# Performance work log

Hardware: AMD Instinct MI355X
Metric: run time of the kernel (lower is better)

## Reference

```python
import math
import jax, jax.numpy as jnp
import numpy as np

DIM = 256
HEADS = 8
WS = (8, 8)   # window_size
SS = (4, 4)   # shift_size


def _rel_tables():
    """Static SwinV2 continuous relative-position coordinate table and index."""
    wh, ww = WS
    ch = np.arange(-(wh - 1), wh, dtype=np.float32)
    cw = np.arange(-(ww - 1), ww, dtype=np.float32)
    table = np.stack(np.meshgrid(ch, cw, indexing='ij'), axis=-1)  # (2wh-1, 2ww-1, 2)
    table[..., 0] /= (wh - 1)
    table[..., 1] /= (ww - 1)
    table *= 8.0
    table = np.sign(table) * np.log2(np.abs(table) + 1.0) / 3.0
    coords = np.stack(np.meshgrid(np.arange(wh), np.arange(ww), indexing='ij'))
    cf = coords.reshape(2, -1)                      # (2, N)
    rel = (cf[:, :, None] - cf[:, None, :]).transpose(1, 2, 0)  # (N, N, 2)
    rel[..., 0] += wh - 1
    rel[..., 1] += ww - 1
    rel[..., 0] *= 2 * ww - 1
    idx = rel.sum(-1).reshape(-1)                   # (N*N,)
    return jnp.asarray(table, jnp.float32), jnp.asarray(idx, jnp.int32)


def _attn_mask(pad_H, pad_W, sh, sw):
    """Static shifted-window attention mask, shape (num_windows, N, N)."""
    wh, ww = WS
    m = np.zeros((pad_H, pad_W), np.float32)
    cnt = 0
    for hs in ((0, -wh), (-wh, -sh), (-sh, None)):
        for ws_ in ((0, -ww), (-ww, -sw), (-sw, None)):
            m[hs[0]:hs[1], ws_[0]:ws_[1]] = cnt
            cnt += 1
    m = m.reshape(pad_H // wh, wh, pad_W // ww, ww).transpose(0, 2, 1, 3)
    m = m.reshape(-1, wh * ww)                      # (nW, N)
    diff = m[:, None, :] - m[:, :, None]            # (nW, N, N)
    return jnp.asarray(np.where(diff != 0, -100.0, 0.0).astype(np.float32))


def setup_inputs() -> dict:
    key = jax.random.key(0)
    ks = jax.random.split(key, 12)
    C, Hh = DIM, HEADS
    s = 0.02
    inp = {
        'x': jax.random.normal(ks[0], (16, 64, 64, C), jnp.float32),
        'Wq': jax.random.normal(ks[1], (C, C), jnp.float32) * s,
        'bq': jnp.zeros((C,), jnp.float32),
        'Wk': jax.random.normal(ks[2], (C, C), jnp.float32) * s,
        'bk': jnp.zeros((C,), jnp.float32),
        'Wv': jax.random.normal(ks[3], (C, C), jnp.float32) * s,
        'bv': jnp.zeros((C,), jnp.float32),
        'Wo': jax.random.normal(ks[4], (C, C), jnp.float32) * s,
        'bo': jnp.zeros((C,), jnp.float32),
        'logit_scale': jnp.full((Hh, 1, 1), math.log(10.0), jnp.float32),
        'cpb_w1': jax.random.normal(ks[5], (2, 512), jnp.float32) * s,
        'cpb_b1': jnp.zeros((512,), jnp.float32),
        'cpb_w2': jax.random.normal(ks[6], (512, Hh), jnp.float32) * s,
    }
    return inp


def reference(x, Wq, bq, Wk, bk, Wv, bv, Wo, bo, logit_scale, cpb_w1, cpb_b1, cpb_w2):
    B, H, W, C = x.shape
    wh, ww = WS
    hd = C // HEADS
    pad_b = (wh - H % wh) % wh
    pad_r = (ww - W % ww) % ww
    x = jnp.pad(x, ((0, 0), (0, pad_b), (0, pad_r), (0, 0)))
    pH, pW = H + pad_b, W + pad_r
    sh = 0 if wh >= pH else SS[0]
    sw = 0 if ww >= pW else SS[1]

    xs = jnp.roll(x, (-sh, -sw), axis=(1, 2))
    nW = (pH // wh) * (pW // ww)
    N = wh * ww
    # window partition -> (B*nW, N, C)
    xw = xs.reshape(B, pH // wh, wh, pW // ww, ww, C).transpose(0, 1, 3, 2, 4, 5)
    xw = xw.reshape(B * nW, N, C)

    def heads(t):
        return t.reshape(B * nW, N, HEADS, hd).transpose(0, 2, 1, 3)  # (BnW, H, N, hd)

    q = heads(xw @ Wq + bq)
    k = heads(xw @ Wk + bk)
    v = heads(xw @ Wv + bv)

    # cosine attention (F.normalize, eps=1e-12)
    qn = q / jnp.maximum(jnp.linalg.norm(q, axis=-1, keepdims=True), 1e-12)
    kn = k / jnp.maximum(jnp.linalg.norm(k, axis=-1, keepdims=True), 1e-12)
    attn = jnp.einsum('bhnd,bhmd->bhnm', qn, kn)

    scale = jnp.exp(jnp.minimum(logit_scale, math.log(100.0)))  # (HEADS,1,1)
    attn = attn * scale[None]

    table, idx = _rel_tables()
    bias = jax.nn.relu(table @ cpb_w1 + cpb_b1) @ cpb_w2        # (2wh-1, 2ww-1, HEADS)
    bias = bias.reshape(-1, HEADS)[idx].reshape(N, N, HEADS).transpose(2, 0, 1)
    attn = attn + (16.0 * jax.nn.sigmoid(bias))[None]

    if sh + sw > 0:
        mask = _attn_mask(pH, pW, sh, sw)                        # (nW, N, N)
        attn = attn.reshape(B, nW, HEADS, N, N) + mask[None, :, None]
        attn = attn.reshape(B * nW, HEADS, N, N)

    attn = jax.nn.softmax(attn, axis=-1)
    out = jnp.einsum('bhnm,bhmd->bhnd', attn, v)
    out = out.transpose(0, 2, 1, 3).reshape(B * nW, N, C)
    out = out @ Wo + bo

    out = out.reshape(B, pH // wh, pW // ww, wh, ww, C).transpose(0, 1, 3, 2, 4, 5)
    out = out.reshape(B, pH, pW, C)
    if sh + sw > 0:
        out = jnp.roll(out, (sh, sw), axis=(1, 2))
    return out[:, :H, :W, :]
```

## Files before the change

### kernel.cpp

```cpp
#include <hip/hip_runtime.h>
#include <hip/hip_bf16.h>

typedef float floatx4 __attribute__((ext_vector_type(4)));
typedef short shortx8 __attribute__((ext_vector_type(8)));
typedef short shortx4 __attribute__((ext_vector_type(4)));

#define CFENCE() asm volatile("" ::: "memory")

__device__ __forceinline__ float bf2f(short s) {
    union { unsigned u; float f; } cv;
    cv.u = ((unsigned)(unsigned short)s) << 16;
    return cv.f;
}
__device__ __forceinline__ short f2bf(float f) {
    union { float f; unsigned u; } cv; cv.f = f;
    unsigned r = (cv.u + 0x7fffu + ((cv.u >> 16) & 1u)) >> 16;
    return (short)r;
}

__global__ __launch_bounds__(256) void wtrans(const float* __restrict__ Wq,
                                              const float* __restrict__ Wk,
                                              const float* __restrict__ Wv,
                                              const float* __restrict__ Wo,
                                              short* __restrict__ wqkv_f,
                                              short* __restrict__ wo_f) {
    int gtid = blockIdx.x * 256 + threadIdx.x;
    int f = gtid >> 6, lane = gtid & 63;
    int quad = lane >> 4, l15 = lane & 15;
    if (f < 384) {
        int n16 = f >> 3, kt = f & 7;
        int n = n16 * 16 + l15, z = n >> 8, ncol = n & 255;
        const float* src = (z == 0) ? Wq : (z == 1) ? Wk : Wv;
        shortx8 s;
#pragma unroll
        for (int j = 0; j < 8; ++j)
            s[j] = f2bf(src[(size_t)(kt * 32 + quad * 8 + j) * 256 + ncol]);
        *(shortx8*)(wqkv_f + (size_t)f * 512 + lane * 8) = s;
    } else {
        int f2 = f - 384;
        int n16 = f2 >> 3, kt = f2 & 7;
        int n = n16 * 16 + l15;
        shortx8 s;
#pragma unroll
        for (int j = 0; j < 8; ++j)
            s[j] = f2bf(Wo[(size_t)(kt * 32 + quad * 8 + j) * 256 + n]);
        *(shortx8*)(wo_f + (size_t)f2 * 512 + lane * 8) = s;
    }
}

__device__ __forceinline__ float sgnlog(float x) {
    return copysignf(__log2f(fabsf(x) + 1.f) / 3.f, x);
}
__global__ __launch_bounds__(256) void bias_mlp(const float* __restrict__ ls,
                                                const float* __restrict__ w1,
                                                const float* __restrict__ b1,
                                                const float* __restrict__ w2,
                                                float* __restrict__ b225g,
                                                float* __restrict__ scaleOut) {
    int e = blockIdx.x;
    int tid = threadIdx.x, lane = tid & 63, wid = tid >> 6;
    if (e == 0 && tid < 8) scaleOut[tid] = expf(fminf(ls[tid], 4.6051701859880914f));
    int dh = e / 15 - 7, dw = e % 15 - 7;
    float t0 = sgnlog(8.f * (float)dh / 7.f);
    float t1 = sgnlog(8.f * (float)dw / 7.f);
    float acc[8];
#pragma unroll
    for (int j = 0; j < 8; ++j) acc[j] = 0.f;
#pragma unroll
    for (int s = 0; s < 2; ++s) {
        int hsm = tid + s * 256;
        float hid = fmaxf(0.f, t0 * w1[hsm] + t1 * w1[512 + hsm] + b1[hsm]);
#pragma unroll
        for (int j = 0; j < 8; ++j) acc[j] += hid * w2[hsm * 8 + j];
    }
#pragma unroll
    for (int off = 1; off < 64; off <<= 1)
#pragma unroll
        for (int j = 0; j < 8; ++j) acc[j] += __shfl_xor(acc[j], off, 64);
    __shared__ float red[4][8];
    if (lane == 0)
#pragma unroll
        for (int j = 0; j < 8; ++j) red[wid][j] = acc[j];
    __syncthreads();
    if (tid < 8)
        b225g[e * 8 + tid] = red[0][tid] + red[1][tid] + red[2][tid] + red[3][tid];
}

__global__ __launch_bounds__(256) void bias_expand(const float* __restrict__ b225g,
                                                   float* __restrict__ bias_t) {
    int f = blockIdx.x * 256 + threadIdx.x;
    int h = f >> 12, ij = f & 4095, i = ij >> 6, j = ij & 63;
    int dh = (i >> 3) - (j >> 3), dw = (i & 7) - (j & 7);
    int e = (dh + 7) * 15 + (dw + 7);
    float v = b225g[e * 8 + h];
    bias_t[(h << 12) + j * 64 + i] = 16.f / (1.f + expf(-v));
}

__device__ __forceinline__ int row2pix(int row) {
    int w = row >> 6, t = row & 63;
    int b = w >> 6, wi = (w >> 3) & 7, wj = w & 7;
    int hh = (wi * 8 + (t >> 3) + 4) & 63;
    int ww = (wj * 8 + (t & 7) + 4) & 63;
    return (b * 64 + hh) * 64 + ww;
}

__device__ __forceinline__ int regid(int t, int wi, int wj) {
    int a = (wi < 7) ? 0 : (((t >> 3) < 4) ? 1 : 2);
    int b = (wj < 7) ? 0 : (((t & 7) < 4) ? 1 : 2);
    return a * 3 + b;
}

__global__ __launch_bounds__(256) void xtrans(const float* __restrict__ x,
                                              short* __restrict__ xbf) {
    int win = blockIdx.x;
    int tid = threadIdx.x;
    int r = tid >> 2, q = tid & 3;
    const float* src = x + (size_t)row2pix(win * 64 + r) * 256 + q * 64;
    size_t fb = (size_t)(win * 4 + (r >> 4)) * 8;
    int l15r = r & 15;
#pragma unroll
    for (int kt2 = 0; kt2 < 2; ++kt2) {
        int kt = q * 2 + kt2;
        short* dst = xbf + (fb + kt) * 512 + l15r * 8;
#pragma unroll
        for (int quad = 0; quad < 4; ++quad) {
            float4 u0 = *(const float4*)(src + kt2 * 32 + quad * 8);
            float4 u1 = *(const float4*)(src + kt2 * 32 + quad * 8 + 4);
            shortx8 t;
            t[0] = f2bf(u0.x); t[1] = f2bf(u0.y); t[2] = f2bf(u0.z); t[3] = f2bf(u0.w);
            t[4] = f2bf(u1.x); t[5] = f2bf(u1.y); t[6] = f2bf(u1.z); t[7] = f2bf(u1.w);
            *(shortx8*)(dst + quad * 128) = t;
        }
    }
}

__global__ __launch_bounds__(256, 2) void swin_fused(const short* __restrict__ xbf,
                                                     const short* __restrict__ wf,
                                                     const short* __restrict__ wof,
                                                     const float* __restrict__ bq,
                                                     const float* __restrict__ bk_,
                                                     const float* __restrict__ bv,
                                                     const float* __restrict__ bo,
                                                     const float* __restrict__ bias_t,
                                                     const float* __restrict__ scale,
                                                     float* __restrict__ out) {
    __shared__ __align__(16) short lds[26112];
    int tid = threadIdx.x, lane = tid & 63, wid = tid >> 6;
    int quad = lane >> 4, l15 = lane & 15;
    int win = blockIdx.x;
    int wi = (win >> 3) & 7, wj = win & 7;
    bool need_mask = (wi == 7) || (wj == 7);

    short* qn = &lds[wid * 6528];
    short* kn = qn + 2176;
    short* vt = qn + 4352;
    short* P  = qn;

    const short* xfb = xbf + (size_t)(win * 4) * 8 * 512 + lane * 8;

    shortx4 Obf[2][4][2];

#pragma unroll
    for (int p = 0; p < 2; ++p) {
        int h = wid * 2 + p;
        float sc = scale[h];
        floatx4 aq[2][4], ak[2][4];
#pragma unroll
        for (int i = 0; i < 2; ++i)
#pragma unroll
            for (int mt = 0; mt < 4; ++mt) {
                aq[i][mt] = (floatx4){0.f, 0.f, 0.f, 0.f};
                ak[i][mt] = (floatx4){0.f, 0.f, 0.f, 0.f};
            }
#pragma unroll
        for (int kt = 0; kt < 8; ++kt) {
            shortx8 af[4];
#pragma unroll
            for (int mt = 0; mt < 4; ++mt)
                af[mt] = *(const shortx8*)(xfb + (size_t)(mt * 8 + kt) * 512);
            shortx8 wqf[2], wkf[2];
#pragma unroll
            for (int i = 0; i < 2; ++i) {
                int n16 = 2 * h + i;
                wqf[i] = *(const shortx8*)(wf + (size_t)((n16)*8 + kt) * 512 + lane * 8);
                wkf[i] = *(const shortx8*)(wf + (size_t)((16 + n16) * 8 + kt) * 512 + lane * 8);
            }
#pragma unroll
            for (int i = 0; i < 2; ++i)
#pragma unroll
                for (int mt = 0; mt < 4; ++mt) {
                    aq[i][mt] = __builtin_amdgcn_mfma_f32_16x16x32_bf16(wqf[i], af[mt], aq[i][mt], 0, 0, 0);
                    ak[i][mt] = __builtin_amdgcn_mfma_f32_16x16x32_bf16(wkf[i], af[mt], ak[i][mt], 0, 0, 0);
                }
        }
        float qs[4], ks[4];
#pragma unroll
        for (int mt = 0; mt < 4; ++mt) { qs[mt] = 0.f; ks[mt] = 0.f; }
#pragma unroll
        for (int i = 0; i < 2; ++i) {
            float bqv[4], bkv[4];
#pragma unroll
            for (int r = 0; r < 4; ++r) {
                int d = i * 16 + quad * 4 + r;
                bqv[r] = bq[h * 32 + d];
                bkv[r] = bk_[h * 32 + d];
            }
#pragma unroll
            for (int mt = 0; mt < 4; ++mt)
#pragma unroll
                for (int r = 0; r < 4; ++r) {
                    float qv = aq[i][mt][r] + bqv[r]; aq[i][mt][r] = qv; qs[mt] += qv * qv;
                    float kv = ak[i][mt][r] + bkv[r]; ak[i][mt][r] = kv; ks[mt] += kv * kv;
                }
        }
#pragma unroll
        for (int mt = 0; mt < 4; ++mt) {
            qs[mt] += __shfl_xor(qs[mt], 16, 64); qs[mt] += __shfl_xor(qs[mt], 32, 64);
            ks[mt] += __shfl_xor(ks[mt], 16, 64); ks[mt] += __shfl_xor(ks[mt], 32, 64);
        }
        CFENCE();
#pragma unroll
        for (int mt = 0; mt < 4; ++mt) {
            float qr = sc / fmaxf(sqrtf(qs[mt]), 1e-12f);
            float kr = 1.f / fmaxf(sqrtf(ks[mt]), 1e-12f);
            int tok = mt * 16 + l15;
#pragma unroll
            for (int i = 0; i < 2; ++i) {
                shortx4 oq, ok;
#pragma unroll
                for (int r = 0; r < 4; ++r) {
                    oq[r] = f2bf(aq[i][mt][r] * qr);
                    ok[r] = f2bf(ak[i][mt][r] * kr);
                }
                *(shortx4*)&qn[tok * 34 + i * 16 + quad * 4] = oq;
                *(shortx4*)&kn[tok * 34 + i * 16 + quad * 4] = ok;
            }
        }
        CFENCE();
        floatx4 av[2][4];
#pragma unroll
        for (int i = 0; i < 2; ++i)
#pragma unroll
            for (int mt = 0; mt < 4; ++mt) av[i][mt] = (floatx4){0.f, 0.f, 0.f, 0.f};
#pragma unroll
        for (int kt = 0; kt < 8; ++kt) {
            shortx8 af[4];
#pragma unroll
            for (int mt = 0; mt < 4; ++mt)
                af[mt] = *(const shortx8*)(xfb + (size_t)(mt * 8 + kt) * 512);
            shortx8 wvf[2];
#pragma unroll
            for (int i = 0; i < 2; ++i) {
                int n16 = 2 * h + i;
                wvf[i] = *(const shortx8*)(wf + (size_t)((32 + n16) * 8 + kt) * 512 + lane * 8);
            }
#pragma unroll
            for (int i = 0; i < 2; ++i)
#pragma unroll
                for (int mt = 0; mt < 4; ++mt)
                    av[i][mt] = __builtin_amdgcn_mfma_f32_16x16x32_bf16(wvf[i], af[mt], av[i][mt], 0, 0, 0);
        }
#pragma unroll
        for (int i = 0; i < 2; ++i) {
            float bvv[4];
#pragma unroll
            for (int r = 0; r < 4; ++r) bvv[r] = bv[h * 32 + i * 16 + quad * 4 + r];
#pragma unroll
            for (int mt = 0; mt < 4; ++mt) {
                int tok = mt * 16 + l15;
#pragma unroll
                for (int r = 0; r < 4; ++r)
                    vt[(i * 16 + quad * 4 + r) * 68 + tok] = f2bf(av[i][mt][r] + bvv[r]);
            }
        }
        CFENCE();
        shortx8 aqf[4], bkf[4];
#pragma unroll
        for (int mt = 0; mt < 4; ++mt)
            aqf[mt] = *(const shortx8*)&qn[(mt * 16 + l15) * 34 + quad * 8];
#pragma unroll
        for (int nt = 0; nt < 4; ++nt)
            bkf[nt] = *(const shortx8*)&kn[(nt * 16 + l15) * 34 + quad * 8];
        floatx4 S[4][4];
#pragma unroll
        for (int mt = 0; mt < 4; ++mt)
#pragma unroll
            for (int nt = 0; nt < 4; ++nt) {
                floatx4 z = {0.f, 0.f, 0.f, 0.f};
                S[mt][nt] = __builtin_amdgcn_mfma_f32_16x16x32_bf16(aqf[mt], bkf[nt], z, 0, 0, 0);
            }
        const float* bh = bias_t + (h << 12);
        float bound = sc + 16.5f;
        int jid[4];
        if (need_mask) {
#pragma unroll
            for (int nt = 0; nt < 4; ++nt) jid[nt] = regid(nt * 16 + l15, wi, wj);
        }
        float rs[4][4];
#pragma unroll
        for (int mt = 0; mt < 4; ++mt) {
            float4 b4[4];
#pragma unroll
            for (int nt = 0; nt < 4; ++nt)
                b4[nt] = *(const float4*)&bh[(nt * 16 + l15) * 64 + mt * 16 + quad * 4];
#pragma unroll
            for (int reg = 0; reg < 4; ++reg) {
                int i = mt * 16 + quad * 4 + reg;
                int iid = need_mask ? regid(i, wi, wj) : 0;
                float rowsum = 0.f;
#pragma unroll
                for (int nt = 0; nt < 4; ++nt) {
                    float bb = (reg == 0) ? b4[nt].x : (reg == 1) ? b4[nt].y
                             : (reg == 2) ? b4[nt].z : b4[nt].w;
                    float v = S[mt][nt][reg] + bb;
                    if (need_mask && iid != jid[nt]) v -= 100.f;
                    float pe = __expf(v - bound);
                    S[mt][nt][reg] = pe;
                    rowsum += pe;
                }
                rowsum += __shfl_xor(rowsum, 1, 64);
                rowsum += __shfl_xor(rowsum, 2, 64);
                rowsum += __shfl_xor(rowsum, 4, 64);
                rowsum += __shfl_xor(rowsum, 8, 64);
                rs[mt][reg] = 1.f / rowsum;
            }
        }
        CFENCE();
#pragma unroll
        for (int mt = 0; mt < 4; ++mt)
#pragma unroll
            for (int nt = 0; nt < 4; ++nt)
#pragma unroll
                for (int reg = 0; reg < 4; ++reg)
                    P[(mt * 16 + quad * 4 + reg) * 68 + nt * 16 + l15] = f2bf(S[mt][nt][reg]);
        CFENCE();
        floatx4 O[4][2];
#pragma unroll
        for (int mt = 0; mt < 4; ++mt)
#pragma unroll
            for (int nt = 0; nt < 2; ++nt) O[mt][nt] = (floatx4){0.f, 0.f, 0.f, 0.f};
#pragma unroll
        for (int ks2 = 0; ks2 < 2; ++ks2) {
            shortx8 pa[4], vb[2];
#pragma unroll
            for (int mt = 0; mt < 4; ++mt)
                pa[mt] = *(const shortx8*)&P[(mt * 16 + l15) * 68 + ks2 * 32 + quad * 8];
#pragma unroll
            for (int nt = 0; nt < 2; ++nt)
                vb[nt] = *(const shortx8*)&vt[(nt * 16 + l15) * 68 + ks2 * 32 + quad * 8];
#pragma unroll
            for (int mt = 0; mt < 4; ++mt)
#pragma unroll
                for (int nt = 0; nt < 2; ++nt)
                    O[mt][nt] = __builtin_amdgcn_mfma_f32_16x16x32_bf16(pa[mt], vb[nt], O[mt][nt], 0, 0, 0);
        }
#pragma unroll
        for (int mt = 0; mt < 4; ++mt)
#pragma unroll
            for (int nt = 0; nt < 2; ++nt) {
                shortx4 s;
#pragma unroll
                for (int reg = 0; reg < 4; ++reg)
                    s[reg] = f2bf(O[mt][nt][reg] * rs[mt][reg]);
                Obf[p][mt][nt] = s;
            }
        CFENCE();
    }

    __syncthreads();
    short* Ao = lds;
#pragma unroll
    for (int p = 0; p < 2; ++p) {
        int h = wid * 2 + p;
#pragma unroll
        for (int mt = 0; mt < 4; ++mt)
#pragma unroll
            for (int nt = 0; nt < 2; ++nt)
#pragma unroll
                for (int reg = 0; reg < 4; ++reg)
                    Ao[(mt * 16 + quad * 4 + reg) * 264 + h * 32 + nt * 16 + l15] =
                        Obf[p][mt][nt][reg];
    }
    __syncthreads();

    int pix[4];
#pragma unroll
    for (int mt = 0; mt < 4; ++mt) pix[mt] = row2pix(win * 64 + mt * 16 + l15);

    floatx4 acc2[4][4];
#pragma unroll
    for (int nt = 0; nt < 4; ++nt)
#pragma unroll
        for (int mt = 0; mt < 4; ++mt) acc2[nt][mt] = (floatx4){0.f, 0.f, 0.f, 0.f};
#pragma unroll
    for (int kt = 0; kt < 8; ++kt) {
        shortx8 bw[4], af2[4];
#pragma unroll
        for (int nt = 0; nt < 4; ++nt)
            bw[nt] = *(const shortx8*)(wof + (size_t)((wid * 4 + nt) * 8 + kt) * 512 + lane * 8);
#pragma unroll
        for (int mt = 0; mt < 4; ++mt)
            af2[mt] = *(const shortx8*)&Ao[(mt * 16 + l15) * 264 + kt * 32 + quad * 8];
#pragma unroll
        for (int nt = 0; nt < 4; ++nt)
#pragma unroll
            for (int mt = 0; mt < 4; ++mt)
                acc2[nt][mt] = __builtin_amdgcn_mfma_f32_16x16x32_bf16(bw[nt], af2[mt], acc2[nt][mt], 0, 0, 0);
    }
#pragma unroll
    for (int nt = 0; nt < 4; ++nt) {
        int nb = wid * 64 + nt * 16 + quad * 4;
        float bs[4];
#pragma unroll
        for (int reg = 0; reg < 4; ++reg) bs[reg] = bo[nb + reg];
#pragma unroll
        for (int mt = 0; mt < 4; ++mt) {
            float4 o;
            o.x = acc2[nt][mt][0] + bs[0];
            o.y = acc2[nt][mt][1] + bs[1];
            o.z = acc2[nt][mt][2] + bs[2];
            o.w = acc2[nt][mt][3] + bs[3];
            *(float4*)(out + (size_t)pix[mt] * 256 + nb) = o;
        }
    }
}

extern "C" void kernel_launch(void* const* d_in, const int* in_sizes, int n_in,
                              void* d_out, int out_size, void* d_ws, size_t ws_size,
                              hipStream_t stream) {
    const float* x  = (const float*)d_in[0];
    const float* Wq = (const float*)d_in[1];
    const float* bq = (const float*)d_in[2];
    const float* Wk = (const float*)d_in[3];
    const float* bk = (const float*)d_in[4];
    const float* Wv = (const float*)d_in[5];
    const float* bv = (const float*)d_in[6];
    const float* Wo = (const float*)d_in[7];
    const float* bo = (const float*)d_in[8];
    const float* ls = (const float*)d_in[9];
    const float* w1 = (const float*)d_in[10];
    const float* b1 = (const float*)d_in[11];
    const float* w2 = (const float*)d_in[12];

    char* ws = (char*)d_ws;
    short* wqkv_f = (short*)(ws + 0);
    short* wo_f   = (short*)(ws + 393216);
    float* bias_t = (float*)(ws + 524288);
    float* scale  = (float*)(ws + 655360);
    float* b225g  = (float*)(ws + 786432);
    short* xbf    = (short*)(ws + 1048576);
    float* out    = (float*)d_out;

    hipLaunchKernelGGL(wtrans, dim3(128), dim3(256), 0, stream, Wq, Wk, Wv, Wo, wqkv_f, wo_f);
    hipLaunchKernelGGL(bias_mlp, dim3(225), dim3(256), 0, stream, ls, w1, b1, w2, b225g, scale);
    hipLaunchKernelGGL(bias_expand, dim3(128), dim3(256), 0, stream, b225g, bias_t);
    hipLaunchKernelGGL(xtrans, dim3(1024), dim3(256), 0, stream, x, xbf);
    hipLaunchKernelGGL(swin_fused, dim3(1024), dim3(256), 0, stream,
                       xbf, wqkv_f, wo_f, bq, bk, bv, bo, bias_t, scale, out);
}
```

Measured before the change: 241.0 us.

## Fuse x bf16 conversion into attention kernel and use one wave per head

```diff
diff --git a/kernel.cpp b/kernel.cpp
--- a/kernel.cpp
+++ b/kernel.cpp
@@ -110,31 +110,7 @@
     return a * 3 + b;
 }
 
-__global__ __launch_bounds__(256) void xtrans(const float* __restrict__ x,
-                                              short* __restrict__ xbf) {
-    int win = blockIdx.x;
-    int tid = threadIdx.x;
-    int r = tid >> 2, q = tid & 3;
-    const float* src = x + (size_t)row2pix(win * 64 + r) * 256 + q * 64;
-    size_t fb = (size_t)(win * 4 + (r >> 4)) * 8;
-    int l15r = r & 15;
-#pragma unroll
-    for (int kt2 = 0; kt2 < 2; ++kt2) {
-        int kt = q * 2 + kt2;
-        short* dst = xbf + (fb + kt) * 512 + l15r * 8;
-#pragma unroll
-        for (int quad = 0; quad < 4; ++quad) {
-            float4 u0 = *(const float4*)(src + kt2 * 32 + quad * 8);
-            float4 u1 = *(const float4*)(src + kt2 * 32 + quad * 8 + 4);
-            shortx8 t;
-            t[0] = f2bf(u0.x); t[1] = f2bf(u0.y); t[2] = f2bf(u0.z); t[3] = f2bf(u0.w);
-            t[4] = f2bf(u1.x); t[5] = f2bf(u1.y); t[6] = f2bf(u1.z); t[7] = f2bf(u1.w);
-            *(shortx8*)(dst + quad * 128) = t;
-        }
-    }
-}
-
-__global__ __launch_bounds__(256, 2) void swin_fused(const short* __restrict__ xbf,
+__global__ __launch_bounds__(512, 2) void swin_fused(const float* __restrict__ x,
                                                      const short* __restrict__ wf,
                                                      const short* __restrict__ wof,
                                                      const float* __restrict__ bq,
@@ -144,272 +120,279 @@
                                                      const float* __restrict__ bias_t,
                                                      const float* __restrict__ scale,
                                                      float* __restrict__ out) {
-    __shared__ __align__(16) short lds[26112];
+    __shared__ __align__(16) short lds[68608];
     int tid = threadIdx.x, lane = tid & 63, wid = tid >> 6;
     int quad = lane >> 4, l15 = lane & 15;
     int win = blockIdx.x;
     int wi = (win >> 3) & 7, wj = win & 7;
     bool need_mask = (wi == 7) || (wj == 7);
 
-    short* qn = &lds[wid * 6528];
+    short* xtile = lds;
+    short* qn = &lds[16384 + wid * 6528];
     short* kn = qn + 2176;
     short* vt = qn + 4352;
     short* P  = qn;
 
-    const short* xfb = xbf + (size_t)(win * 4) * 8 * 512 + lane * 8;
-
-    shortx4 Obf[2][4][2];
-
-#pragma unroll
-    for (int p = 0; p < 2; ++p) {
-        int h = wid * 2 + p;
-        float sc = scale[h];
-        floatx4 aq[2][4], ak[2][4];
+    {
+        int r = tid >> 3, seg = tid & 7;
+        const float* src = x + (size_t)row2pix(win * 64 + r) * 256 + seg * 32;
+        short* dst = &xtile[((r >> 4) * 8 + seg) * 512 + (r & 15) * 8];
+#pragma unroll
+        for (int c4 = 0; c4 < 4; ++c4) {
+            float4 u0 = *(const float4*)(src + c4 * 8);
+            float4 u1 = *(const float4*)(src + c4 * 8 + 4);
+            shortx8 t;
+            t[0] = f2bf(u0.x); t[1] = f2bf(u0.y); t[2] = f2bf(u0.z); t[3] = f2bf(u0.w);
+            t[4] = f2bf(u1.x); t[5] = f2bf(u1.y); t[6] = f2bf(u1.z); t[7] = f2bf(u1.w);
+            *(shortx8*)(dst + c4 * 128) = t;
+        }
+    }
+    __syncthreads();
+
+    int h = wid;
+    float sc = scale[h];
+
+    floatx4 aq[2][4], ak[2][4];
+#pragma unroll
+    for (int i = 0; i < 2; ++i)
+#pragma unroll
+        for (int mt = 0; mt < 4; ++mt) {
+            aq[i][mt] = (floatx4){0.f, 0.f, 0.f, 0.f};
+            ak[i][mt] = (floatx4){0.f, 0.f, 0.f, 0.f};
+        }
+#pragma unroll
+    for (int kt = 0; kt < 8; ++kt) {
+        shortx8 af[4];
+#pragma unroll
+        for (int mt = 0; mt < 4; ++mt)
+            af[mt] = *(const shortx8*)&xtile[(mt * 8 + kt) * 512 + lane * 8];
+        shortx8 wqf[2], wkf[2];
+#pragma unroll
+        for (int i = 0; i < 2; ++i) {
+            int n16 = 2 * h + i;
+            wqf[i] = *(const shortx8*)(wf + (size_t)((n16)*8 + kt) * 512 + lane * 8);
+            wkf[i] = *(const shortx8*)(wf + (size_t)((16 + n16) * 8 + kt) * 512 + lane * 8);
+        }
 #pragma unroll
         for (int i = 0; i < 2; ++i)
 #pragma unroll
             for (int mt = 0; mt < 4; ++mt) {
-                aq[i][mt] = (floatx4){0.f, 0.f, 0.f, 0.f};
-                ak[i][mt] = (floatx4){0.f, 0.f, 0.f, 0.f};
+                aq[i][mt] = __builtin_amdgcn_mfma_f32_16x16x32_bf16(wqf[i], af[mt], aq[i][mt], 0, 0, 0);
+                ak[i][mt] = __builtin_amdgcn_mfma_f32_16x16x32_bf16(wkf[i], af[mt], ak[i][mt], 0, 0, 0);
             }
-#pragma unroll
-        for (int kt = 0; kt < 8; ++kt) {
-            shortx8 af[4];
+    }
+    float qs[4], ks[4];
+#pragma unroll
+    for (int mt = 0; mt < 4; ++mt) { qs[mt] = 0.f; ks[mt] = 0.f; }
+#pragma unroll
+    for (int i = 0; i < 2; ++i) {
+        float bqv[4], bkv[4];
+#pragma unroll
+        for (int r = 0; r < 4; ++r) {
+            int d = i * 16 + quad * 4 + r;
+            bqv[r] = bq[h * 32 + d];
+            bkv[r] = bk_[h * 32 + d];
+        }
+#pragma unroll
+        for (int mt = 0; mt < 4; ++mt)
+#pragma unroll
+            for (int r = 0; r < 4; ++r) {
+                float qv = aq[i][mt][r] + bqv[r]; aq[i][mt][r] = qv; qs[mt] += qv * qv;
+                float kv = ak[i][mt][r] + bkv[r]; ak[i][mt][r] = kv; ks[mt] += kv * kv;
+            }
+    }
+#pragma unroll
+    for (int mt = 0; mt < 4; ++mt) {
+        qs[mt] += __shfl_xor(qs[mt], 16, 64); qs[mt] += __shfl_xor(qs[mt], 32, 64);
+        ks[mt] += __shfl_xor(ks[mt], 16, 64); ks[mt] += __shfl_xor(ks[mt], 32, 64);
+    }
+    CFENCE();
+#pragma unroll
+    for (int mt = 0; mt < 4; ++mt) {
+        float qr = sc / fmaxf(sqrtf(qs[mt]), 1e-12f);
+        float kr = 1.f / fmaxf(sqrtf(ks[mt]), 1e-12f);
+        int tok = mt * 16 + l15;
+#pragma unroll
+        for (int i = 0; i < 2; ++i) {
+            shortx4 oq, ok;
+#pragma unroll
+            for (int r = 0; r < 4; ++r) {
+                oq[r] = f2bf(aq[i][mt][r] * qr);
+                ok[r] = f2bf(ak[i][mt][r] * kr);
+            }
+            *(shortx4*)&qn[tok * 34 + i * 16 + quad * 4] = oq;
+            *(shortx4*)&kn[tok * 34 + i * 16 + quad * 4] = ok;
+        }
+    }
+    CFENCE();
+    floatx4 av[2][4];
+#pragma unroll
+    for (int i = 0; i < 2; ++i)
+#pragma unroll
+        for (int mt = 0; mt < 4; ++mt) av[i][mt] = (floatx4){0.f, 0.f, 0.f, 0.f};
+#pragma unroll
+    for (int kt = 0; kt < 8; ++kt) {
+        shortx8 af[4];
+#pragma unroll
+        for (int mt = 0; mt < 4; ++mt)
+            af[mt] = *(const shortx8*)&xtile[(mt * 8 + kt) * 512 + lane * 8];
+        shortx8 wvf[2];
+#pragma unroll
+        for (int i = 0; i < 2; ++i) {
+            int n16 = 2 * h + i;
+            wvf[i] = *(const shortx8*)(wf + (size_t)((32 + n16) * 8 + kt) * 512 + lane * 8);
+        }
+#pragma unroll
+        for (int i = 0; i < 2; ++i)
 #pragma unroll
             for (int mt = 0; mt < 4; ++mt)
-                af[mt] = *(const shortx8*)(xfb + (size_t)(mt * 8 + kt) * 512);
-            shortx8 wqf[2], wkf[2];
-#pragma unroll
-            for (int i = 0; i < 2; ++i) {
-                int n16 = 2 * h + i;
-                wqf[i] = *(const shortx8*)(wf + (size_t)((n16)*8 + kt) * 512 + lane * 8);
-                wkf[i] = *(const shortx8*)(wf + (size_t)((16 + n16) * 8 + kt) * 512 + lane * 8);
+                av[i][mt] = __builtin_amdgcn_mfma_f32_16x16x32_bf16(wvf[i], af[mt], av[i][mt], 0, 0, 0);
+    }
+#pragma unroll
+    for (int i = 0; i < 2; ++i) {
+        float bvv[4];
+#pragma unroll
+        for (int r = 0; r < 4; ++r) bvv[r] = bv[h * 32 + i * 16 + quad * 4 + r];
+#pragma unroll
+        for (int mt = 0; mt < 4; ++mt) {
+            int tok = mt * 16 + l15;
+#pragma unroll
+            for (int r = 0; r < 4; ++r)
+                vt[(i * 16 + quad * 4 + r) * 68 + tok] = f2bf(av[i][mt][r] + bvv[r]);
+        }
+    }
+    CFENCE();
+    shortx8 aqf[4], bkf[4];
+#pragma unroll
+    for (int mt = 0; mt < 4; ++mt)
+        aqf[mt] = *(const shortx8*)&qn[(mt * 16 + l15) * 34 + quad * 8];
+#pragma unroll
+    for (int nt = 0; nt < 4; ++nt)
+        bkf[nt] = *(const shortx8*)&kn[(nt * 16 + l15) * 34 + quad * 8];
+    floatx4 S[4][4];
+#pragma unroll
+    for (int mt = 0; mt < 4; ++mt)
+#pragma unroll
+        for (int nt = 0; nt < 4; ++nt) {
+            floatx4 z = {0.f, 0.f, 0.f, 0.f};
+            S[mt][nt] = __builtin_amdgcn_mfma_f32_16x16x32_bf16(aqf[mt], bkf[nt], z, 0, 0, 0);
+        }
+    const float* bh = bias_t + (h << 12);
+    float bound = sc + 16.5f;
+    int jid[4];
+    if (need_mask) {
+#pragma unroll
+        for (int nt = 0; nt < 4; ++nt) jid[nt] = regid(nt * 16 + l15, wi, wj);
+    }
+    float rs[4][4];
+#pragma unroll
+    for (int mt = 0; mt < 4; ++mt) {
+        float4 b4[4];
+#pragma unroll
+        for (int nt = 0; nt < 4; ++nt)
+            b4[nt] = *(const float4*)&bh[(nt * 16 + l15) * 64 + mt * 16 + quad * 4];
+#pragma unroll
+        for (int reg = 0; reg < 4; ++reg) {
+            int i = mt * 16 + quad * 4 + reg;
+            int iid = need_mask ? regid(i, wi, wj) : 0;
+            float rowsum = 0.f;
+#pragma unroll
+            for (int nt = 0; nt < 4; ++nt) {
+                float bb = (reg == 0) ? b4[nt].x : (reg == 1) ? b4[nt].y
+                         : (reg == 2) ? b4[nt].z : b4[nt].w;
+                float v = S[mt][nt][reg] + bb;
+                if (need_mask && iid != jid[nt]) v -= 100.f;
+                float pe = __expf(v - bound);
+                S[mt][nt][reg] = pe;
+                rowsum += pe;
             }
-#pragma unroll
-            for (int i = 0; i < 2; ++i)
-#pragma unroll
-                for (int mt = 0; mt < 4; ++mt) {
-                    aq[i][mt] = __builtin_amdgcn_mfma_f32_16x16x32_bf16(wqf[i], af[mt], aq[i][mt], 0, 0, 0);
-                    ak[i][mt] = __builtin_amdgcn_mfma_f32_16x16x32_bf16(wkf[i], af[mt], ak[i][mt], 0, 0, 0);
-                }
-        }
-        float qs[4], ks[4];
-#pragma unroll
-        for (int mt = 0; mt < 4; ++mt) { qs[mt] = 0.f; ks[mt] = 0.f; }
-#pragma unroll
-        for (int i = 0; i < 2; ++i) {
-            float bqv[4], bkv[4];
-#pragma unroll
-            for (int r = 0; r < 4; ++r) {
-                int d = i * 16 + quad * 4 + r;
-                bqv[r] = bq[h * 32 + d];
-                bkv[r] = bk_[h * 32 + d];
-            }
-#pragma unroll
-            for (int mt = 0; mt < 4; ++mt)
-#pragma unroll
-                for (int r = 0; r < 4; ++r) {
-                    float qv = aq[i][mt][r] + bqv[r]; aq[i][mt][r] = qv; qs[mt] += qv * qv;
-                    float kv = ak[i][mt][r] + bkv[r]; ak[i][mt][r] = kv; ks[mt] += kv * kv;
-                }
-        }
-#pragma unroll
-        for (int mt = 0; mt < 4; ++mt) {
-            qs[mt] += __shfl_xor(qs[mt], 16, 64); qs[mt] += __shfl_xor(qs[mt], 32, 64);
-            ks[mt] += __shfl_xor(ks[mt], 16, 64); ks[mt] += __shfl_xor(ks[mt], 32, 64);
-        }
-        CFENCE();
-#pragma unroll
-        for (int mt = 0; mt < 4; ++mt) {
-            float qr = sc / fmaxf(sqrtf(qs[mt]), 1e-12f);
-            float kr = 1.f / fmaxf(sqrtf(ks[mt]), 1e-12f);
-            int tok = mt * 16 + l15;
-#pragma unroll
-            for (int i = 0; i < 2; ++i) {
-                shortx4 oq, ok;
-#pragma unroll
-                for (int r = 0; r < 4; ++r) {
-                    oq[r] = f2bf(aq[i][mt][r] * qr);
-                    ok[r] = f2bf(ak[i][mt][r] * kr);
-                }
-                *(shortx4*)&qn[tok * 34 + i * 16 + quad * 4] = oq;
-                *(shortx4*)&kn[tok * 34 + i * 16 + quad * 4] = ok;
-            }
-        }
-        CFENCE();
-        floatx4 av[2][4];
-#pragma unroll
-        for (int i = 0; i < 2; ++i)
-#pragma unroll
-            for (int mt = 0; mt < 4; ++mt) av[i][mt] = (floatx4){0.f, 0.f, 0.f, 0.f};
-#pragma unroll
-        for (int kt = 0; kt < 8; ++kt) {
-            shortx8 af[4];
-#pragma unroll
-            for (int mt = 0; mt < 4; ++mt)
-                af[mt] = *(const shortx8*)(xfb + (size_t)(mt * 8 + kt) * 512);
-            shortx8 wvf[2];
-#pragma unroll
-            for (int i = 0; i < 2; ++i) {
-                int n16 = 2 * h + i;
-                wvf[i] = *(const shortx8*)(wf + (size_t)((32 + n16) * 8 + kt) * 512 + lane * 8);
-            }
-#pragma unroll
-            for (int i = 0; i < 2; ++i)
-#pragma unroll
-                for (int mt = 0; mt < 4; ++mt)
-                    av[i][mt] = __builtin_amdgcn_mfma_f32_16x16x32_bf16(wvf[i], af[mt], av[i][mt], 0, 0, 0);
-        }
-#pragma unroll
-        for (int i = 0; i < 2; ++i) {
-            float bvv[4];
-#pragma unroll
-            for (int r = 0; r < 4; ++r) bvv[r] = bv[h * 32 + i * 16 + quad * 4 + r];
-#pragma unroll
-            for (int mt = 0; mt < 4; ++mt) {
-                int tok = mt * 16 + l15;
-#pragma unroll
-                for (int r = 0; r < 4; ++r)
-                    vt[(i * 16 + quad * 4 + r) * 68 + tok] = f2bf(av[i][mt][r] + bvv[r]);
-            }
-        }
-        CFENCE();
-        shortx8 aqf[4], bkf[4];
-#pragma unroll
-        for (int mt = 0; mt < 4; ++mt)
-            aqf[mt] = *(const shortx8*)&qn[(mt * 16 + l15) * 34 + quad * 8];
+            rowsum += __shfl_xor(rowsum, 1, 64);
+            rowsum += __shfl_xor(rowsum, 2, 64);
+            rowsum += __shfl_xor(rowsum, 4, 64);
+            rowsum += __shfl_xor(rowsum, 8, 64);
+            rs[mt][reg] = 1.f / rowsum;
+        }
+    }
+    CFENCE();
+#pragma unroll
+    for (int mt = 0; mt < 4; ++mt)
 #pragma unroll
         for (int nt = 0; nt < 4; ++nt)
-            bkf[nt] = *(const shortx8*)&kn[(nt * 16 + l15) * 34 + quad * 8];
-        floatx4 S[4][4];
-#pragma unroll
-        for (int mt = 0; mt < 4; ++mt)
-#pragma unroll
-            for (int nt = 0; nt < 4; ++nt) {
-                floatx4 z = {0.f, 0.f, 0.f, 0.f};
-                S[mt][nt] = __builtin_amdgcn_mfma_f32_16x16x32_bf16(aqf[mt], bkf[nt], z, 0, 0, 0);
-            }
-        const float* bh = bias_t + (h << 12);
-        float bound = sc + 16.5f;
-        int jid[4];
-        if (need_mask) {
-#pragma unroll
-            for (int nt = 0; nt < 4; ++nt) jid[nt] = regid(nt * 16 + l15, wi, wj);
-        }
-        float rs[4][4];
-#pragma unroll
-        for (int mt = 0; mt < 4; ++mt) {
-            float4 b4[4];
-#pragma unroll
-            for (int nt = 0; nt < 4; ++nt)
-                b4[nt] = *(const float4*)&bh[(nt * 16 + l15) * 64 + mt * 16 + quad * 4];
-#pragma unroll
-            for (int reg = 0; reg < 4; ++reg) {
-                int i = mt * 16 + quad * 4 + reg;
-                int iid = need_mask ? regid(i, wi, wj) : 0;
-                float rowsum = 0.f;
-#pragma unroll
-                for (int nt = 0; nt < 4; ++nt) {
-                    float bb = (reg == 0) ? b4[nt].x : (reg == 1) ? b4[nt].y
-                             : (reg == 2) ? b4[nt].z : b4[nt].w;
-                    float v = S[mt][nt][reg] + bb;
-                    if (need_mask && iid != jid[nt]) v -= 100.f;
-                    float pe = __expf(v - bound);
-                    S[mt][nt][reg] = pe;
-                    rowsum += pe;
-                }
-                rowsum += __shfl_xor(rowsum, 1, 64);
-                rowsum += __shfl_xor(rowsum, 2, 64);
-                rowsum += __shfl_xor(rowsum, 4, 64);
-                rowsum += __shfl_xor(rowsum, 8, 64);
-                rs[mt][reg] = 1.f / rowsum;
-            }
-        }
-        CFENCE();
-#pragma unroll
-        for (int mt = 0; mt < 4; ++mt)
-#pragma unroll
-            for (int nt = 0; nt < 4; ++nt)
-#pragma unroll
-                for (int reg = 0; reg < 4; ++reg)
-                    P[(mt * 16 + quad * 4 + reg) * 68 + nt * 16 + l15] = f2bf(S[mt][nt][reg]);
-        CFENCE();
-        floatx4 O[4][2];
-#pragma unroll
-        for (int mt = 0; mt < 4; ++mt)
-#pragma unroll
-            for (int nt = 0; nt < 2; ++nt) O[mt][nt] = (floatx4){0.f, 0.f, 0.f, 0.f};
-#pragma unroll
-        for (int ks2 = 0; ks2 < 2; ++ks2) {
-            shortx8 pa[4], vb[2];
-#pragma unroll
-            for (int mt = 0; mt < 4; ++mt)
-                pa[mt] = *(const shortx8*)&P[(mt * 16 + l15) * 68 + ks2 * 32 + quad * 8];
+#pragma unroll
+            for (int reg = 0; reg < 4; ++reg)
+                P[(mt * 16 + quad * 4 + reg) * 68 + nt * 16 + l15] = f2bf(S[mt][nt][reg]);
+    CFENCE();
+    floatx4 O[4][2];
+#pragma unroll
+    for (int mt = 0; mt < 4; ++mt)
+#pragma unroll
+        for (int nt = 0; nt < 2; ++nt) O[mt][nt] = (floatx4){0.f, 0.f, 0.f, 0.f};
+#pragma unroll
+    for (int ks2 = 0; ks2 < 2; ++ks2) {
+        shortx8 pa[4], vb[2];
+#pragma unroll
+        for (int mt = 0; mt < 4; ++mt)
+            pa[mt] = *(const shortx8*)&P[(mt * 16 + l15) * 68 + ks2 * 32 + quad * 8];
+#pragma unroll
+        for (int nt = 0; nt < 2; ++nt)
+            vb[nt] = *(const shortx8*)&vt[(nt * 16 + l15) * 68 + ks2 * 32 + quad * 8];
+#pragma unroll
+        for (int mt = 0; mt < 4; ++mt)
 #pragma unroll
             for (int nt = 0; nt < 2; ++nt)
-                vb[nt] = *(const shortx8*)&vt[(nt * 16 + l15) * 68 + ks2 * 32 + quad * 8];
-#pragma unroll
-            for (int mt = 0; mt < 4; ++mt)
-#pragma unroll
-                for (int nt = 0; nt < 2; ++nt)
-                    O[mt][nt] = __builtin_amdgcn_mfma_f32_16x16x32_bf16(pa[mt], vb[nt], O[mt][nt], 0, 0, 0);
-        }
-#pragma unroll
-        for (int mt = 0; mt < 4; ++mt)
-#pragma unroll
-            for (int nt = 0; nt < 2; ++nt) {
-                shortx4 s;
-#pragma unroll
-                for (int reg = 0; reg < 4; ++reg)
-                    s[reg] = f2bf(O[mt][nt][reg] * rs[mt][reg]);
-                Obf[p][mt][nt] = s;
-            }
-        CFENCE();
-    }
+                O[mt][nt] = __builtin_amdgcn_mfma_f32_16x16x32_bf16(pa[mt], vb[nt], O[mt][nt], 0, 0, 0);
+    }
+    shortx4 Obf[4][2];
+#pragma unroll
+    for (int mt = 0; mt < 4; ++mt)
+#pragma unroll
+        for (int nt = 0; nt < 2; ++nt) {
+            shortx4 s;
+#pragma unroll
+            for (int reg = 0; reg < 4; ++reg)
+                s[reg] = f2bf(O[mt][nt][reg] * rs[mt][reg]);
+            Obf[mt][nt] = s;
+        }
 
     __syncthreads();
     short* Ao = lds;
 #pragma unroll
-    for (int p = 0; p < 2; ++p) {
-        int h = wid * 2 + p;
-#pragma unroll
-        for (int mt = 0; mt < 4; ++mt)
-#pragma unroll
-            for (int nt = 0; nt < 2; ++nt)
-#pragma unroll
-                for (int reg = 0; reg < 4; ++reg)
-                    Ao[(mt * 16 + quad * 4 + reg) * 264 + h * 32 + nt * 16 + l15] =
-                        Obf[p][mt][nt][reg];
-    }
+    for (int mt = 0; mt < 4; ++mt)
+#pragma unroll
+        for (int nt = 0; nt < 2; ++nt)
+#pragma unroll
+            for (int reg = 0; reg < 4; ++reg)
+                Ao[(mt * 16 + quad * 4 + reg) * 264 + h * 32 + nt * 16 + l15] =
+                    Obf[mt][nt][reg];
     __syncthreads();
 
     int pix[4];
 #pragma unroll
     for (int mt = 0; mt < 4; ++mt) pix[mt] = row2pix(win * 64 + mt * 16 + l15);
 
-    floatx4 acc2[4][4];
-#pragma unroll
-    for (int nt = 0; nt < 4; ++nt)
+    floatx4 acc2[2][4];
+#pragma unroll
+    for (int nt = 0; nt < 2; ++nt)
 #pragma unroll
         for (int mt = 0; mt < 4; ++mt) acc2[nt][mt] = (floatx4){0.f, 0.f, 0.f, 0.f};
 #pragma unroll
     for (int kt = 0; kt < 8; ++kt) {
-        shortx8 bw[4], af2[4];
-#pragma unroll
-        for (int nt = 0; nt < 4; ++nt)
-            bw[nt] = *(const shortx8*)(wof + (size_t)((wid * 4 + nt) * 8 + kt) * 512 + lane * 8);
+        shortx8 bw[2], af2[4];
+#pragma unroll
+        for (int nt = 0; nt < 2; ++nt)
+            bw[nt] = *(const shortx8*)(wof + (size_t)((wid * 2 + nt) * 8 + kt) * 512 + lane * 8);
 #pragma unroll
         for (int mt = 0; mt < 4; ++mt)
             af2[mt] = *(const shortx8*)&Ao[(mt * 16 + l15) * 264 + kt * 32 + quad * 8];
 #pragma unroll
-        for (int nt = 0; nt < 4; ++nt)
+        for (int nt = 0; nt < 2; ++nt)
 #pragma unroll
             for (int mt = 0; mt < 4; ++mt)
                 acc2[nt][mt] = __builtin_amdgcn_mfma_f32_16x16x32_bf16(bw[nt], af2[mt], acc2[nt][mt], 0, 0, 0);
     }
 #pragma unroll
-    for (int nt = 0; nt < 4; ++nt) {
-        int nb = wid * 64 + nt * 16 + quad * 4;
+    for (int nt = 0; nt < 2; ++nt) {
+        int nb = (wid * 2 + nt) * 16 + quad * 4;
         float bs[4];
 #pragma unroll
         for (int reg = 0; reg < 4; ++reg) bs[reg] = bo[nb + reg];
@@ -448,13 +431,11 @@
     float* bias_t = (float*)(ws + 524288);
     float* scale  = (float*)(ws + 655360);
     float* b225g  = (float*)(ws + 786432);
-    short* xbf    = (short*)(ws + 1048576);
     float* out    = (float*)d_out;
 
     hipLaunchKernelGGL(wtrans, dim3(128), dim3(256), 0, stream, Wq, Wk, Wv, Wo, wqkv_f, wo_f);
     hipLaunchKernelGGL(bias_mlp, dim3(225), dim3(256), 0, stream, ls, w1, b1, w2, b225g, scale);
     hipLaunchKernelGGL(bias_expand, dim3(128), dim3(256), 0, stream, b225g, bias_t);
-    hipLaunchKernelGGL(xtrans, dim3(1024), dim3(256), 0, stream, x, xbf);
-    hipLaunchKernelGGL(swin_fused, dim3(1024), dim3(256), 0, stream,
-                       xbf, wqkv_f, wo_f, bq, bk, bv, bo, bias_t, scale, out);
-}
+    hipLaunchKernelGGL(swin_fused, dim3(1024), dim3(512), 0, stream,
+                       x, wqkv_f, wo_f, bq, bk, bv, bo, bias_t, scale, out);
+}
```

Result: faster. 225.9 us (-6.3%).
